# Performance work log

Measured on AMD Instinct MI355X. Metric: run time of the kernel, lower is better.

The kernel has to match this reference:

```python
import jax, jax.numpy as jnp
import numpy as np

GROUP = 128  # int4 quant group size and Hadamard block size

# Sylvester Hadamard matrix of size 128, orthonormal (H @ H.T = I)
_h = np.array([[1.0]], dtype=np.float32)
while _h.shape[0] < GROUP:
    _h = np.kron(_h, np.array([[1.0, 1.0], [1.0, -1.0]], dtype=np.float32))
H128 = jnp.asarray(_h / np.sqrt(GROUP))


def hadamard_rotate(x):
    # blockwise Hadamard rotation along the last dim (last dim % 128 == 0)
    *lead, n = x.shape
    xr = x.reshape(*lead, n // GROUP, GROUP) @ H128
    return xr.reshape(*lead, n)


def dequant_int4(wq, scales):
    # wq: [out, in] uint4 values in [0,16); scales: [out, in//GROUP]
    out_dim, in_dim = wq.shape
    w = (wq.astype(jnp.float32) - 8.0).reshape(out_dim, in_dim // GROUP, GROUP)
    w = w * scales[:, :, None]
    return w.reshape(out_dim, in_dim)


def rotate_linear_int4(x, wq, scales):
    # y = hadamard(x) @ dequant(W).T
    return hadamard_rotate(x) @ dequant_int4(wq, scales).T


def setup_inputs() -> dict:
    key = jax.random.key(0)
    ks = jax.random.split(key, 7)
    T, D, I = 4096, 4096, 12288  # tokens, hidden, intermediate
    x = jax.random.normal(ks[0], (T, D), dtype=jnp.float32)
    wq_gate = jax.random.randint(ks[1], (I, D), 0, 16, dtype=jnp.int32)
    s_gate = jax.random.uniform(ks[2], (I, D // GROUP), dtype=jnp.float32) * 0.01
    wq_up = jax.random.randint(ks[3], (I, D), 0, 16, dtype=jnp.int32)
    s_up = jax.random.uniform(ks[4], (I, D // GROUP), dtype=jnp.float32) * 0.01
    wq_down = jax.random.randint(ks[5], (D, I), 0, 16, dtype=jnp.int32)
    s_down = jax.random.uniform(ks[6], (D, I // GROUP), dtype=jnp.float32) * 0.01
    return {"x": x, "wq_gate": wq_gate, "s_gate": s_gate,
            "wq_up": wq_up, "s_up": s_up,
            "wq_down": wq_down, "s_down": s_down}


def reference(x, wq_gate, s_gate, wq_up, s_up, wq_down, s_down):
    gate = rotate_linear_int4(x, wq_gate, s_gate)   # [T, I]
    up = rotate_linear_int4(x, wq_up, s_up)         # [T, I]
    h = jax.nn.silu(gate) * up                       # SiluAndMul on cat([gate, up])
    return rotate_linear_int4(h, wq_down, s_down)    # [T, D]
```

## Files before the change

### kernel.cpp

```cpp
#include <hip/hip_runtime.h>
#include <hip/hip_bf16.h>
#include <cstdint>

#define T_DIM 4096
#define D_DIM 4096
#define I_DIM 12288
#define GRP   128

typedef __attribute__((ext_vector_type(8))) short bf16x8;
typedef __attribute__((ext_vector_type(4))) float f32x4;
typedef __attribute__((ext_vector_type(4))) int   int32x4;

typedef __attribute__((address_space(3))) void lds_void;
typedef const __attribute__((address_space(1))) void gmem_void;

static __device__ __forceinline__ unsigned short f2bf(float f) {
    unsigned int u = __float_as_uint(f);
    u += 0x7FFFu + ((u >> 16) & 1u);
    return (unsigned short)(u >> 16);
}
static __device__ __forceinline__ float bf2f(unsigned short b) {
    return __uint_as_float(((unsigned int)b) << 16);
}

__global__ void had_f32_to_bf16(const float* __restrict__ in, unsigned short* __restrict__ out,
                                int ngroups) {
    int gid = blockIdx.x * (blockDim.x >> 6) + (threadIdx.x >> 6);
    if (gid >= ngroups) return;
    int lane = threadIdx.x & 63;
    const float2 v2 = *reinterpret_cast<const float2*>(in + (size_t)gid * 128 + lane * 2);
    float v0 = v2.x, v1 = v2.y;
    { float t0 = v0 + v1, t1 = v0 - v1; v0 = t0; v1 = t1; }
#pragma unroll
    for (int m = 1; m <= 32; m <<= 1) {
        float b0 = __shfl_xor(v0, m);
        float b1 = __shfl_xor(v1, m);
        if (lane & m) { v0 = b0 - v0; v1 = b1 - v1; }
        else          { v0 = v0 + b0; v1 = v1 + b1; }
    }
    const float s = 0.08838834764831843f;
    unsigned int o = (unsigned int)f2bf(v0 * s) | ((unsigned int)f2bf(v1 * s) << 16);
    *reinterpret_cast<unsigned int*>(out + (size_t)gid * 128 + lane * 2) = o;
}

__global__ void had_bf16_inplace(unsigned short* __restrict__ buf, int ngroups) {
    int gid = blockIdx.x * (blockDim.x >> 6) + (threadIdx.x >> 6);
    if (gid >= ngroups) return;
    int lane = threadIdx.x & 63;
    unsigned int pv = *reinterpret_cast<const unsigned int*>(buf + (size_t)gid * 128 + lane * 2);
    float v0 = __uint_as_float((pv & 0xFFFFu) << 16);
    float v1 = __uint_as_float(pv & 0xFFFF0000u);
    { float t0 = v0 + v1, t1 = v0 - v1; v0 = t0; v1 = t1; }
#pragma unroll
    for (int m = 1; m <= 32; m <<= 1) {
        float b0 = __shfl_xor(v0, m);
        float b1 = __shfl_xor(v1, m);
        if (lane & m) { v0 = b0 - v0; v1 = b1 - v1; }
        else          { v0 = v0 + b0; v1 = v1 + b1; }
    }
    const float s = 0.08838834764831843f;
    unsigned int o = (unsigned int)f2bf(v0 * s) | ((unsigned int)f2bf(v1 * s) << 16);
    *reinterpret_cast<unsigned int*>(buf + (size_t)gid * 128 + lane * 2) = o;
}

__global__ void dequant_w(const int* __restrict__ Wq, const float* __restrict__ S,
                          unsigned short* __restrict__ Wbf, int In, int total8) {
    int t = blockIdx.x * blockDim.x + threadIdx.x;
    if (t >= total8) return;
    size_t base = (size_t)t * 8;
    size_t row = base / (size_t)In;
    int col = (int)(base - row * (size_t)In);
    float sc = S[row * (size_t)(In >> 7) + (col >> 7)];
    const int32x4* p = reinterpret_cast<const int32x4*>(Wq + base);
    int32x4 a = p[0], b = p[1];
    float nsc = -8.0f * sc;
    unsigned int o0 = (unsigned int)f2bf((float)a.x * sc + nsc) |
                      ((unsigned int)f2bf((float)a.y * sc + nsc) << 16);
    unsigned int o1 = (unsigned int)f2bf((float)a.z * sc + nsc) |
                      ((unsigned int)f2bf((float)a.w * sc + nsc) << 16);
    unsigned int o2 = (unsigned int)f2bf((float)b.x * sc + nsc) |
                      ((unsigned int)f2bf((float)b.y * sc + nsc) << 16);
    unsigned int o3 = (unsigned int)f2bf((float)b.z * sc + nsc) |
                      ((unsigned int)f2bf((float)b.w * sc + nsc) << 16);
    *reinterpret_cast<uint4*>(Wbf + base) = make_uint4(o0, o1, o2, o3);
}


#define GBAR()  __builtin_amdgcn_s_barrier()
#define LGKM0() asm volatile("s_waitcnt lgkmcnt(0)" ::: "memory")
#define VMW(n)  asm volatile("s_waitcnt vmcnt(" #n ")" ::: "memory")
#define P1()    __builtin_amdgcn_s_setprio(1)
#define P0()    __builtin_amdgcn_s_setprio(0)

#define STG(bb, mat, h, kb)                                                            \
  { _Pragma("unroll")                                                                  \
    for (int i_ = 0; i_ < 2; ++i_) {                                                   \
      const int rl_ = (h) * 128 + i_ * 64 + (tid >> 3);                                \
      const int gs_ = (tid & 7) ^ ((tid >> 3) & 7);                                    \
      const unsigned short* gp_ = ((mat) ? W : A) +                                    \
          (size_t)(((mat) ? n0 : m0) + rl_) * K + (kb) + gs_ * 8;                      \
      unsigned short* lp_ = lds + (bb) * 32768 + (mat) * 16384 +                       \
          ((h) * 128 + i_ * 64 + wid * 8) * 64;                                        \
      __builtin_amdgcn_global_load_lds((gmem_void*)gp_, (lds_void*)lp_, 16, 0, 0);     \
    } }

#define LDA(bb, q)                                                                     \
  _Pragma("unroll")                                                                    \
  for (int mi_ = 0; mi_ < 2; ++mi_)                                                    \
  _Pragma("unroll")                                                                    \
  for (int ks_ = 0; ks_ < 2; ++ks_) {                                                  \
    int r_ = wr * 128 + ((q) * 2 + mi_) * 16 + (lane & 15);                            \
    int c_ = ks_ * 4 + kc;                                                             \
    af[mi_][ks_] = *reinterpret_cast<const bf16x8*>(                                   \
        lds + (bb) * 32768 + r_ * 64 + ((c_ ^ (r_ & 7)) << 3));                        \
  }

#define LDB(bb)                                                                        \
  _Pragma("unroll")                                                                    \
  for (int ni_ = 0; ni_ < 4; ++ni_)                                                    \
  _Pragma("unroll")                                                                    \
  for (int ks_ = 0; ks_ < 2; ++ks_) {                                                  \
    int r_ = wc * 64 + ni_ * 16 + (lane & 15);                                         \
    int c_ = ks_ * 4 + kc;                                                             \
    bk[ni_][ks_] = *reinterpret_cast<const bf16x8*>(                                   \
        lds + (bb) * 32768 + 16384 + r_ * 64 + ((c_ ^ (r_ & 7)) << 3));                \
  }

#define MF16(q)                                                                        \
  _Pragma("unroll")                                                                    \
  for (int ks_ = 0; ks_ < 2; ++ks_)                                                    \
  _Pragma("unroll")                                                                    \
  for (int mi_ = 0; mi_ < 2; ++mi_)                                                    \
  _Pragma("unroll")                                                                    \
  for (int ni_ = 0; ni_ < 4; ++ni_)                                                    \
    acc[(q) * 2 + mi_][ni_] = __builtin_amdgcn_mfma_f32_16x16x32_bf16(                 \
        af[mi_][ks_], bk[ni_][ks_], acc[(q) * 2 + mi_][ni_], 0, 0, 0);

template<int MODE>
__global__ __launch_bounds__(512, 2)
void gemm256(const unsigned short* __restrict__ A,
             const unsigned short* __restrict__ W,
             void* __restrict__ C, int M, int N, int K)
{
    __shared__ __align__(16) unsigned short lds[65536];

    const int MT = M >> 8;
    const int nwg = gridDim.x;
    const int bid = blockIdx.x;
    const int cpx = nwg >> 3;
    const int wg  = (bid & 7) * cpx + (bid >> 3);
    const int m0 = (wg % MT) << 8;
    const int n0 = (wg / MT) << 8;

    const int tid  = threadIdx.x;
    const int lane = tid & 63;
    const int wid  = tid >> 6;
    const int wr = wid >> 2;
    const int wc = wid & 3;
    const int kc = lane >> 4;

    f32x4 acc[8][4];
#pragma unroll
    for (int i = 0; i < 8; ++i)
#pragma unroll
        for (int j = 0; j < 4; ++j) acc[i][j] = (f32x4)0.0f;

    const int NT = K >> 6;
    const int J  = NT >> 1;

    STG(0, 0, 0, 0); STG(0, 0, 1, 0); STG(0, 1, 0, 0); STG(0, 1, 1, 0);
    STG(1, 1, 0, 64); STG(1, 1, 1, 64);
    VMW(4);
    GBAR();

    bf16x8 af[2][2], bk[4][2];

    for (int j = 0; j < J - 1; ++j) {
        const int ka  = (j << 7);
        const int kb1 = ka + 64;
        const int ka2 = ka + 128;
        const int ka3 = ka + 192;
        LDB(0); LDA(0, 0); STG(1, 0, 0, kb1);
        GBAR(); LGKM0(); P1(); MF16(0); P0(); GBAR();
        LDA(0, 1); STG(1, 0, 1, kb1);
        GBAR(); LGKM0(); P1(); MF16(1); P0(); GBAR();
        LDA(0, 2); STG(0, 1, 0, ka2);
        GBAR(); LGKM0(); P1(); MF16(2); P0(); GBAR();
        LDA(0, 3); STG(0, 1, 1, ka2);
        GBAR(); LGKM0(); P1(); MF16(3); P0(); VMW(4); GBAR();
        LDB(1); LDA(1, 0); STG(0, 0, 0, ka2);
        GBAR(); LGKM0(); P1(); MF16(0); P0(); GBAR();
        LDA(1, 1); STG(0, 0, 1, ka2);
        GBAR(); LGKM0(); P1(); MF16(1); P0(); GBAR();
        LDA(1, 2); STG(1, 1, 0, ka3);
        GBAR(); LGKM0(); P1(); MF16(2); P0(); GBAR();
        LDA(1, 3); STG(1, 1, 1, ka3);
        GBAR(); LGKM0(); P1(); MF16(3); P0(); VMW(4); GBAR();
    }

    {
        const int kb1 = ((NT - 1) << 6);
        LDB(0); LDA(0, 0); STG(1, 0, 0, kb1);
        GBAR(); LGKM0(); P1(); MF16(0); P0(); GBAR();
        LDA(0, 1); STG(1, 0, 1, kb1);
        GBAR(); LGKM0(); P1(); MF16(1); P0(); GBAR();
        LDA(0, 2);
        GBAR(); LGKM0(); P1(); MF16(2); P0(); GBAR();
        LDA(0, 3);
        GBAR(); LGKM0(); P1(); MF16(3); P0(); VMW(0); GBAR();
        LDB(1); LDA(1, 0);
        GBAR(); LGKM0(); P1(); MF16(0); P0(); GBAR();
        LDA(1, 1);
        GBAR(); LGKM0(); P1(); MF16(1); P0(); GBAR();
        LDA(1, 2);
        GBAR(); LGKM0(); P1(); MF16(2); P0(); GBAR();
        LDA(1, 3);
        GBAR(); LGKM0(); P1(); MF16(3); P0(); GBAR();
    }

#pragma unroll
    for (int mi = 0; mi < 8; ++mi)
#pragma unroll
        for (int ni = 0; ni < 4; ++ni) {
            const int col = n0 + (wc << 6) + ni * 16 + (lane & 15);
#pragma unroll
            for (int r = 0; r < 4; ++r) {
                const int row = m0 + (wr << 7) + mi * 16 + ((lane >> 4) << 2) + r;
                const size_t idx = (size_t)row * N + col;
                if (MODE == 2) {
                    ((float*)C)[idx] = acc[mi][ni][r];
                } else if (MODE == 0) {
                    ((unsigned short*)C)[idx] = f2bf(acc[mi][ni][r]);
                } else {
                    float g = bf2f(((unsigned short*)C)[idx]);
                    float u = acc[mi][ni][r];
                    float h = (g / (1.0f + __expf(-g))) * u;
                    ((unsigned short*)C)[idx] = f2bf(h);
                }
            }
        }
}

__global__ __launch_bounds__(256, 2)
void gemm_gateup_fb(const unsigned short* __restrict__ Xr,
                    const int* __restrict__ Wg, const float* __restrict__ Sg,
                    const int* __restrict__ Wu, const float* __restrict__ Su,
                    unsigned short* __restrict__ H)
{
    __shared__ __align__(16) unsigned short lA [128 * 64];
    __shared__ __align__(16) unsigned short lBg[128 * 64];
    __shared__ __align__(16) unsigned short lBu[128 * 64];
    const int MT = T_DIM / 128;
    const int bid = blockIdx.x;
    const int m0 = (bid % MT) * 128;
    const int n0 = (bid / MT) * 128;
    const int tid  = threadIdx.x;
    const int lane = tid & 63;
    const int wid  = tid >> 6;
    const int wr = wid >> 1, wc = wid & 1;
    f32x4 accG[4][4], accU[4][4];
#pragma unroll
    for (int i = 0; i < 4; ++i)
#pragma unroll
        for (int j = 0; j < 4; ++j) { accG[i][j] = (f32x4)0.0f; accU[i][j] = (f32x4)0.0f; }
    const int arow = lane >> 3;
    const int acol = (lane & 7) * 8;
    const int SStride = D_DIM / GRP;
    for (int k0 = 0; k0 < D_DIM; k0 += 64) {
        __syncthreads();
#pragma unroll
        for (int it = 0; it < 4; ++it) {
            int chunk = wid * 4 + it;
            const unsigned short* gp = Xr + (size_t)(m0 + chunk * 8 + arow) * D_DIM + k0 + acol;
            __builtin_amdgcn_global_load_lds((gmem_void*)gp, (lds_void*)(lA + chunk * 512), 16, 0, 0);
        }
        const int g = k0 >> 7;
#pragma unroll
        for (int i = 0; i < 8; ++i) {
            int linear = i * 1024 + tid * 4;
            int r = linear >> 6;
            int c = linear & 63;
            const int32x4 wg = *reinterpret_cast<const int32x4*>(Wg + (size_t)(n0 + r) * D_DIM + k0 + c);
            const int32x4 wu = *reinterpret_cast<const int32x4*>(Wu + (size_t)(n0 + r) * D_DIM + k0 + c);
            float scg = Sg[(size_t)(n0 + r) * SStride + g];
            float scu = Su[(size_t)(n0 + r) * SStride + g];
            unsigned int g01 = (unsigned int)f2bf((float)(wg.x - 8) * scg) | ((unsigned int)f2bf((float)(wg.y - 8) * scg) << 16);
            unsigned int g23 = (unsigned int)f2bf((float)(wg.z - 8) * scg) | ((unsigned int)f2bf((float)(wg.w - 8) * scg) << 16);
            unsigned int u01 = (unsigned int)f2bf((float)(wu.x - 8) * scu) | ((unsigned int)f2bf((float)(wu.y - 8) * scu) << 16);
            unsigned int u23 = (unsigned int)f2bf((float)(wu.z - 8) * scu) | ((unsigned int)f2bf((float)(wu.w - 8) * scu) << 16);
            *reinterpret_cast<uint2*>(lBg + r * 64 + c) = make_uint2(g01, g23);
            *reinterpret_cast<uint2*>(lBu + r * 64 + c) = make_uint2(u01, u23);
        }
        __syncthreads();
#pragma unroll
        for (int ks = 0; ks < 2; ++ks) {
            const int koff = ks * 32 + (lane >> 4) * 8;
            bf16x8 af[4], bg[4], bu[4];
#pragma unroll
            for (int mi = 0; mi < 4; ++mi)
                af[mi] = *reinterpret_cast<const bf16x8*>(lA + (wr * 64 + mi * 16 + (lane & 15)) * 64 + koff);
#pragma unroll
            for (int ni = 0; ni < 4; ++ni) {
                bg[ni] = *reinterpret_cast<const bf16x8*>(lBg + (wc * 64 + ni * 16 + (lane & 15)) * 64 + koff);
                bu[ni] = *reinterpret_cast<const bf16x8*>(lBu + (wc * 64 + ni * 16 + (lane & 15)) * 64 + koff);
            }
#pragma unroll
            for (int mi = 0; mi < 4; ++mi)
#pragma unroll
                for (int ni = 0; ni < 4; ++ni) {
                    accG[mi][ni] = __builtin_amdgcn_mfma_f32_16x16x32_bf16(af[mi], bg[ni], accG[mi][ni], 0, 0, 0);
                    accU[mi][ni] = __builtin_amdgcn_mfma_f32_16x16x32_bf16(af[mi], bu[ni], accU[mi][ni], 0, 0, 0);
                }
        }
    }
#pragma unroll
    for (int mi = 0; mi < 4; ++mi)
#pragma unroll
        for (int ni = 0; ni < 4; ++ni) {
            const int col = n0 + wc * 64 + ni * 16 + (lane & 15);
#pragma unroll
            for (int r = 0; r < 4; ++r) {
                const int row = m0 + wr * 64 + mi * 16 + (lane >> 4) * 4 + r;
                float gv = accG[mi][ni][r];
                float uv = accU[mi][ni][r];
                float hv = (gv / (1.0f + __expf(-gv))) * uv;
                H[(size_t)row * I_DIM + col] = f2bf(hv);
            }
        }
}

__global__ __launch_bounds__(256, 2)
void gemm_down_fb(const unsigned short* __restrict__ Hr,
                  const int* __restrict__ Wd, const float* __restrict__ Sd,
                  float* __restrict__ Out)
{
    __shared__ __align__(16) unsigned short lA[128 * 64];
    __shared__ __align__(16) unsigned short lB[128 * 64];
    const int MT = T_DIM / 128;
    const int bid = blockIdx.x;
    const int m0 = (bid % MT) * 128;
    const int n0 = (bid / MT) * 128;
    const int tid  = threadIdx.x;
    const int lane = tid & 63;
    const int wid  = tid >> 6;
    const int wr = wid >> 1, wc = wid & 1;
    f32x4 acc[4][4];
#pragma unroll
    for (int i = 0; i < 4; ++i)
#pragma unroll
        for (int j = 0; j < 4; ++j) acc[i][j] = (f32x4)0.0f;
    const int arow = lane >> 3;
    const int acol = (lane & 7) * 8;
    const int SStride = I_DIM / GRP;
    for (int k0 = 0; k0 < I_DIM; k0 += 64) {
        __syncthreads();
#pragma unroll
        for (int it = 0; it < 4; ++it) {
            int chunk = wid * 4 + it;
            const unsigned short* gp = Hr + (size_t)(m0 + chunk * 8 + arow) * I_DIM + k0 + acol;
            __builtin_amdgcn_global_load_lds((gmem_void*)gp, (lds_void*)(lA + chunk * 512), 16, 0, 0);
        }
        const int g = k0 >> 7;
#pragma unroll
        for (int i = 0; i < 8; ++i) {
            int linear = i * 1024 + tid * 4;
            int r = linear >> 6;
            int c = linear & 63;
            const int32x4 wd = *reinterpret_cast<const int32x4*>(Wd + (size_t)(n0 + r) * I_DIM + k0 + c);
            float sc = Sd[(size_t)(n0 + r) * SStride + g];
            unsigned int d01 = (unsigned int)f2bf((float)(wd.x - 8) * sc) | ((unsigned int)f2bf((float)(wd.y - 8) * sc) << 16);
            unsigned int d23 = (unsigned int)f2bf((float)(wd.z - 8) * sc) | ((unsigned int)f2bf((float)(wd.w - 8) * sc) << 16);
            *reinterpret_cast<uint2*>(lB + r * 64 + c) = make_uint2(d01, d23);
        }
        __syncthreads();
#pragma unroll
        for (int ks = 0; ks < 2; ++ks) {
            const int koff = ks * 32 + (lane >> 4) * 8;
            bf16x8 af[4], bfr[4];
#pragma unroll
            for (int mi = 0; mi < 4; ++mi)
                af[mi] = *reinterpret_cast<const bf16x8*>(lA + (wr * 64 + mi * 16 + (lane & 15)) * 64 + koff);
#pragma unroll
            for (int ni = 0; ni < 4; ++ni)
                bfr[ni] = *reinterpret_cast<const bf16x8*>(lB + (wc * 64 + ni * 16 + (lane & 15)) * 64 + koff);
#pragma unroll
            for (int mi = 0; mi < 4; ++mi)
#pragma unroll
                for (int ni = 0; ni < 4; ++ni)
                    acc[mi][ni] = __builtin_amdgcn_mfma_f32_16x16x32_bf16(af[mi], bfr[ni], acc[mi][ni], 0, 0, 0);
        }
    }
#pragma unroll
    for (int mi = 0; mi < 4; ++mi)
#pragma unroll
        for (int ni = 0; ni < 4; ++ni) {
            const int col = n0 + wc * 64 + ni * 16 + (lane & 15);
#pragma unroll
            for (int r = 0; r < 4; ++r) {
                const int row = m0 + wr * 64 + mi * 16 + (lane >> 4) * 4 + r;
                Out[(size_t)row * D_DIM + col] = acc[mi][ni][r];
            }
        }
}

extern "C" void kernel_launch(void* const* d_in, const int* in_sizes, int n_in,
                              void* d_out, int out_size, void* d_ws, size_t ws_size,
                              hipStream_t stream) {
    const float* x       = (const float*)d_in[0];
    const int*   wq_gate = (const int*)d_in[1];
    const float* s_gate  = (const float*)d_in[2];
    const int*   wq_up   = (const int*)d_in[3];
    const float* s_up    = (const float*)d_in[4];
    const int*   wq_down = (const int*)d_in[5];
    const float* s_down  = (const float*)d_in[6];
    float* out = (float*)d_out;

    const size_t XR_E = (size_t)T_DIM * D_DIM;
    const size_t H_E  = (size_t)T_DIM * I_DIM;
    const size_t W_E  = (size_t)I_DIM * D_DIM;
    const size_t need = (XR_E + H_E + 2 * W_E) * sizeof(unsigned short);

    unsigned short* xr = (unsigned short*)d_ws;
    unsigned short* h  = xr + XR_E;

    {
        int ngroups = (int)(XR_E / 128);
        had_f32_to_bf16<<<dim3(ngroups / 4), dim3(256), 0, stream>>>(x, xr, ngroups);
    }

    if (ws_size >= need) {
        unsigned short* wgbf = h + H_E;
        unsigned short* wubf = wgbf + W_E;
        int total8 = (int)(W_E / 8);
        dequant_w<<<dim3((total8 + 255) / 256), dim3(256), 0, stream>>>(wq_gate, s_gate, wgbf, D_DIM, total8);
        dequant_w<<<dim3((total8 + 255) / 256), dim3(256), 0, stream>>>(wq_up,   s_up,   wubf, D_DIM, total8);
        gemm256<0><<<dim3((T_DIM / 256) * (I_DIM / 256)), dim3(512), 0, stream>>>(
            xr, wgbf, (void*)h, T_DIM, I_DIM, D_DIM);
        gemm256<1><<<dim3((T_DIM / 256) * (I_DIM / 256)), dim3(512), 0, stream>>>(
            xr, wubf, (void*)h, T_DIM, I_DIM, D_DIM);
        {
            int ngroups = (int)(H_E / 128);
            had_bf16_inplace<<<dim3(ngroups / 4), dim3(256), 0, stream>>>(h, ngroups);
        }
        dequant_w<<<dim3((total8 + 255) / 256), dim3(256), 0, stream>>>(wq_down, s_down, wgbf, I_DIM, total8);
        gemm256<2><<<dim3((T_DIM / 256) * (D_DIM / 256)), dim3(512), 0, stream>>>(
            h, wgbf, (void*)out, T_DIM, D_DIM, I_DIM);
    } else {
        gemm_gateup_fb<<<dim3((T_DIM / 128) * (I_DIM / 128)), dim3(256), 0, stream>>>(
            xr, wq_gate, s_gate, wq_up, s_up, h);
        {
            int ngroups = (int)(H_E / 128);
            had_bf16_inplace<<<dim3(ngroups / 4), dim3(256), 0, stream>>>(h, ngroups);
        }
        gemm_down_fb<<<dim3((T_DIM / 128) * (D_DIM / 128)), dim3(256), 0, stream>>>(
            h, wq_down, s_down, out);
    }
}
```

Baseline: 1.280 ms.

## Triple-buffer A tiles in LDS and drop explicit lgkmcnt waits in GEMM pipeline

Restructures the bf16 GEMM main loop so the A operand rotates through three LDS buffers while B keeps two, with staging loads issued earlier to deepen the prefetch distance. The explicit lgkmcnt(0) waits and several barriers per sub-step are removed, leaving the compiler to insert LDS waits, and the peeled tail iteration is folded into the loop behind a predicate. LDS use grows from 128KB to 160KB per workgroup, which may cut occupancy below the declared two blocks per CU, and the reduced barrier count raises the risk of LDS reuse races.

```diff
diff --git a/kernel.cpp b/kernel.cpp
--- a/kernel.cpp
+++ b/kernel.cpp
@@ -87,35 +87,33 @@
 
 
 #define GBAR()  __builtin_amdgcn_s_barrier()
-#define LGKM0() asm volatile("s_waitcnt lgkmcnt(0)" ::: "memory")
+#define FENCE() asm volatile("" ::: "memory")
 #define VMW(n)  asm volatile("s_waitcnt vmcnt(" #n ")" ::: "memory")
 #define P1()    __builtin_amdgcn_s_setprio(1)
 #define P0()    __builtin_amdgcn_s_setprio(0)
 
-#define STG(bb, mat, h, kb)                                                            \
+#define STG(src, row0, base, h, kb)                                                    \
   { _Pragma("unroll")                                                                  \
     for (int i_ = 0; i_ < 2; ++i_) {                                                   \
       const int rl_ = (h) * 128 + i_ * 64 + (tid >> 3);                                \
       const int gs_ = (tid & 7) ^ ((tid >> 3) & 7);                                    \
-      const unsigned short* gp_ = ((mat) ? W : A) +                                    \
-          (size_t)(((mat) ? n0 : m0) + rl_) * K + (kb) + gs_ * 8;                      \
-      unsigned short* lp_ = lds + (bb) * 32768 + (mat) * 16384 +                       \
-          ((h) * 128 + i_ * 64 + wid * 8) * 64;                                        \
+      const unsigned short* gp_ = (src) + (size_t)((row0) + rl_) * K + (kb) + gs_ * 8; \
+      unsigned short* lp_ = lds + (base) + ((h) * 128 + i_ * 64 + wid * 8) * 64;       \
       __builtin_amdgcn_global_load_lds((gmem_void*)gp_, (lds_void*)lp_, 16, 0, 0);     \
     } }
 
-#define LDA(bb, q)                                                                     \
+#define LDA(base, q)                                                                   \
   _Pragma("unroll")                                                                    \
   for (int mi_ = 0; mi_ < 2; ++mi_)                                                    \
   _Pragma("unroll")                                                                    \
   for (int ks_ = 0; ks_ < 2; ++ks_) {                                                  \
-    int r_ = wr * 128 + ((q) * 2 + mi_) * 16 + (lane & 15);                            \
+    int r_ = wr * 128 + (q) * 32 + mi_ * 16 + (lane & 15);                             \
     int c_ = ks_ * 4 + kc;                                                             \
     af[mi_][ks_] = *reinterpret_cast<const bf16x8*>(                                   \
-        lds + (bb) * 32768 + r_ * 64 + ((c_ ^ (r_ & 7)) << 3));                        \
+        lds + (base) + r_ * 64 + ((c_ ^ (r_ & 7)) << 3));                              \
   }
 
-#define LDB(bb)                                                                        \
+#define LDB(base)                                                                      \
   _Pragma("unroll")                                                                    \
   for (int ni_ = 0; ni_ < 4; ++ni_)                                                    \
   _Pragma("unroll")                                                                    \
@@ -123,7 +121,7 @@
     int r_ = wc * 64 + ni_ * 16 + (lane & 15);                                         \
     int c_ = ks_ * 4 + kc;                                                             \
     bk[ni_][ks_] = *reinterpret_cast<const bf16x8*>(                                   \
-        lds + (bb) * 32768 + 16384 + r_ * 64 + ((c_ ^ (r_ & 7)) << 3));                \
+        lds + (base) + r_ * 64 + ((c_ ^ (r_ & 7)) << 3));                              \
   }
 
 #define MF16(q)                                                                        \
@@ -135,6 +133,9 @@
   for (int ni_ = 0; ni_ < 4; ++ni_)                                                    \
     acc[(q) * 2 + mi_][ni_] = __builtin_amdgcn_mfma_f32_16x16x32_bf16(                 \
         af[mi_][ks_], bk[ni_][ks_], acc[(q) * 2 + mi_][ni_], 0, 0, 0);
+
+#define B0_ 49152
+#define B1_ 65536
 
 template<int MODE>
 __global__ __launch_bounds__(512, 2)
@@ -142,7 +143,7 @@
              const unsigned short* __restrict__ W,
              void* __restrict__ C, int M, int N, int K)
 {
-    __shared__ __align__(16) unsigned short lds[65536];
+    __shared__ __align__(16) unsigned short lds[81920];
 
     const int MT = M >> 8;
     const int nwg = gridDim.x;
@@ -168,54 +169,53 @@
     const int NT = K >> 6;
     const int J  = NT >> 1;
 
-    STG(0, 0, 0, 0); STG(0, 0, 1, 0); STG(0, 1, 0, 0); STG(0, 1, 1, 0);
-    STG(1, 1, 0, 64); STG(1, 1, 1, 64);
-    VMW(4);
-    GBAR();
-
-    bf16x8 af[2][2], bk[4][2];
-
-    for (int j = 0; j < J - 1; ++j) {
-        const int ka  = (j << 7);
-        const int kb1 = ka + 64;
-        const int ka2 = ka + 128;
-        const int ka3 = ka + 192;
-        LDB(0); LDA(0, 0); STG(1, 0, 0, kb1);
-        GBAR(); LGKM0(); P1(); MF16(0); P0(); GBAR();
-        LDA(0, 1); STG(1, 0, 1, kb1);
-        GBAR(); LGKM0(); P1(); MF16(1); P0(); GBAR();
-        LDA(0, 2); STG(0, 1, 0, ka2);
-        GBAR(); LGKM0(); P1(); MF16(2); P0(); GBAR();
-        LDA(0, 3); STG(0, 1, 1, ka2);
-        GBAR(); LGKM0(); P1(); MF16(3); P0(); VMW(4); GBAR();
-        LDB(1); LDA(1, 0); STG(0, 0, 0, ka2);
-        GBAR(); LGKM0(); P1(); MF16(0); P0(); GBAR();
-        LDA(1, 1); STG(0, 0, 1, ka2);
-        GBAR(); LGKM0(); P1(); MF16(1); P0(); GBAR();
-        LDA(1, 2); STG(1, 1, 0, ka3);
-        GBAR(); LGKM0(); P1(); MF16(2); P0(); GBAR();
-        LDA(1, 3); STG(1, 1, 1, ka3);
-        GBAR(); LGKM0(); P1(); MF16(3); P0(); VMW(4); GBAR();
-    }
-
-    {
-        const int kb1 = ((NT - 1) << 6);
-        LDB(0); LDA(0, 0); STG(1, 0, 0, kb1);
-        GBAR(); LGKM0(); P1(); MF16(0); P0(); GBAR();
-        LDA(0, 1); STG(1, 0, 1, kb1);
-        GBAR(); LGKM0(); P1(); MF16(1); P0(); GBAR();
-        LDA(0, 2);
-        GBAR(); LGKM0(); P1(); MF16(2); P0(); GBAR();
-        LDA(0, 3);
-        GBAR(); LGKM0(); P1(); MF16(3); P0(); VMW(0); GBAR();
-        LDB(1); LDA(1, 0);
-        GBAR(); LGKM0(); P1(); MF16(0); P0(); GBAR();
-        LDA(1, 1);
-        GBAR(); LGKM0(); P1(); MF16(1); P0(); GBAR();
-        LDA(1, 2);
-        GBAR(); LGKM0(); P1(); MF16(2); P0(); GBAR();
-        LDA(1, 3);
-        GBAR(); LGKM0(); P1(); MF16(3); P0(); GBAR();
+    STG(A, m0, 0,     0, 0);  STG(A, m0, 0,     1, 0);
+    STG(W, n0, B0_,   0, 0);  STG(W, n0, B0_,   1, 0);
+    STG(A, m0, 16384, 0, 64); STG(A, m0, 16384, 1, 64);
+    STG(W, n0, B1_,   0, 64);
+    VMW(6);
+    GBAR(); FENCE();
+
+    int ra = 0, rb = 1, rc = 2;
+
+    for (int j = 0; j < J; ++j) {
+        const bool st = (j < J - 1);
+        const int a   = j << 1;
+        const int kT1 = (a + 1) << 6;
+        const int kT2 = (a + 2) << 6;
+        const int kT3 = (a + 3) << 6;
+        const int baA = ra << 14, bbA = rb << 14, bcA = rc << 14;
+        bf16x8 af[2][2], bk[4][2];
+
+        STG(W, n0, B1_, 1, kT1);
+        LDB(B0_); LDA(baA, 0);
+        P1(); MF16(0); P0(); GBAR(); FENCE();
+        if (st) STG(A, m0, bcA, 0, kT2);
+        LDA(baA, 1);
+        P1(); MF16(1); P0(); GBAR(); FENCE();
+        if (st) STG(W, n0, B0_, 0, kT2);
+        LDA(baA, 2);
+        P1(); MF16(2); P0(); GBAR(); FENCE();
+        if (st) STG(W, n0, B0_, 1, kT2);
+        LDA(baA, 3);
+        P1(); MF16(3); P0();
+        if (st) { VMW(6); } else { VMW(0); }
+        GBAR(); FENCE();
+        if (st) STG(A, m0, bcA, 1, kT2);
+        LDB(B1_); LDA(bbA, 0);
+        P1(); MF16(0); P0(); GBAR(); FENCE();
+        if (st) STG(A, m0, baA, 0, kT3);
+        LDA(bbA, 1);
+        P1(); MF16(1); P0(); GBAR(); FENCE();
+        if (st) STG(A, m0, baA, 1, kT3);
+        LDA(bbA, 2);
+        P1(); MF16(2); P0(); GBAR(); FENCE();
+        if (st) STG(W, n0, B1_, 0, kT3);
+        LDA(bbA, 3);
+        P1(); MF16(3); P0();
+        if (st) { VMW(6); }
+        GBAR(); FENCE();
+        int t_ = ra; ra = rc; rc = rb; rb = t_;
     }
 
 #pragma unroll
```

Result: no change. 1.302 ms (+1.7%).

## Double-buffer A fragments in registers to prefetch the next LDS quarter during MFMA

Applied to the files above, without the earlier changes.

The GEMM main loop now keeps two register sets of A fragments and loads the next quarter tile from LDS while the MFMAs for the current quarter run. The explicit lgkmcnt(0) waits are removed, so the compiler's dependency-based waits can let LDS reads overlap with matrix math. The prologue now waits for the first stage and preloads the first A quarter. The vmcnt waits are moved to just before reads of the other LDS buffer. Those reads now come right after the wait with no barrier in between, which risks a race with other waves' async loads, and the extra fragment registers raise register pressure.

```diff
diff --git a/kernel.cpp b/kernel.cpp
--- a/kernel.cpp
+++ b/kernel.cpp
@@ -87,7 +87,6 @@
 
 
 #define GBAR()  __builtin_amdgcn_s_barrier()
-#define LGKM0() asm volatile("s_waitcnt lgkmcnt(0)" ::: "memory")
 #define VMW(n)  asm volatile("s_waitcnt vmcnt(" #n ")" ::: "memory")
 #define P1()    __builtin_amdgcn_s_setprio(1)
 #define P0()    __builtin_amdgcn_s_setprio(0)
@@ -104,18 +103,18 @@
       __builtin_amdgcn_global_load_lds((gmem_void*)gp_, (lds_void*)lp_, 16, 0, 0);     \
     } }
 
-#define LDA(bb, q)                                                                     \
+#define LDAQ(dst, bb, q)                                                               \
   _Pragma("unroll")                                                                    \
   for (int mi_ = 0; mi_ < 2; ++mi_)                                                    \
   _Pragma("unroll")                                                                    \
   for (int ks_ = 0; ks_ < 2; ++ks_) {                                                  \
-    int r_ = wr * 128 + ((q) * 2 + mi_) * 16 + (lane & 15);                            \
+    int r_ = wr * 128 + (q) * 32 + mi_ * 16 + (lane & 15);                             \
     int c_ = ks_ * 4 + kc;                                                             \
-    af[mi_][ks_] = *reinterpret_cast<const bf16x8*>(                                   \
+    dst[mi_][ks_] = *reinterpret_cast<const bf16x8*>(                                  \
         lds + (bb) * 32768 + r_ * 64 + ((c_ ^ (r_ & 7)) << 3));                        \
   }
 
-#define LDB(bb)                                                                        \
+#define LDBQ(bb)                                                                       \
   _Pragma("unroll")                                                                    \
   for (int ni_ = 0; ni_ < 4; ++ni_)                                                    \
   _Pragma("unroll")                                                                    \
@@ -126,7 +125,7 @@
         lds + (bb) * 32768 + 16384 + r_ * 64 + ((c_ ^ (r_ & 7)) << 3));                \
   }
 
-#define MF16(q)                                                                        \
+#define MF16(q, afb)                                                                   \
   _Pragma("unroll")                                                                    \
   for (int ks_ = 0; ks_ < 2; ++ks_)                                                    \
   _Pragma("unroll")                                                                    \
@@ -134,7 +133,7 @@
   _Pragma("unroll")                                                                    \
   for (int ni_ = 0; ni_ < 4; ++ni_)                                                    \
     acc[(q) * 2 + mi_][ni_] = __builtin_amdgcn_mfma_f32_16x16x32_bf16(                 \
-        af[mi_][ks_], bk[ni_][ks_], acc[(q) * 2 + mi_][ni_], 0, 0, 0);
+        afb[mi_][ks_], bk[ni_][ks_], acc[(q) * 2 + mi_][ni_], 0, 0, 0);
 
 template<int MODE>
 __global__ __launch_bounds__(512, 2)
@@ -168,54 +167,55 @@
     const int NT = K >> 6;
     const int J  = NT >> 1;
 
-    STG(0, 0, 0, 0); STG(0, 0, 1, 0); STG(0, 1, 0, 0); STG(0, 1, 1, 0);
+    bf16x8 afA[2][2], afB[2][2], bk[4][2];
+
+    STG(0, 0, 0, 0); STG(0, 0, 1, 0);
+    STG(0, 1, 0, 0); STG(0, 1, 1, 0);
+    VMW(0);
+    GBAR();
+    LDAQ(afA, 0, 0);
     STG(1, 1, 0, 64); STG(1, 1, 1, 64);
-    VMW(4);
-    GBAR();
-
-    bf16x8 af[2][2], bk[4][2];
 
     for (int j = 0; j < J - 1; ++j) {
         const int ka  = (j << 7);
         const int kb1 = ka + 64;
         const int ka2 = ka + 128;
         const int ka3 = ka + 192;
-        LDB(0); LDA(0, 0); STG(1, 0, 0, kb1);
-        GBAR(); LGKM0(); P1(); MF16(0); P0(); GBAR();
-        LDA(0, 1); STG(1, 0, 1, kb1);
-        GBAR(); LGKM0(); P1(); MF16(1); P0(); GBAR();
-        LDA(0, 2); STG(0, 1, 0, ka2);
-        GBAR(); LGKM0(); P1(); MF16(2); P0(); GBAR();
-        LDA(0, 3); STG(0, 1, 1, ka2);
-        GBAR(); LGKM0(); P1(); MF16(3); P0(); VMW(4); GBAR();
-        LDB(1); LDA(1, 0); STG(0, 0, 0, ka2);
-        GBAR(); LGKM0(); P1(); MF16(0); P0(); GBAR();
-        LDA(1, 1); STG(0, 0, 1, ka2);
-        GBAR(); LGKM0(); P1(); MF16(1); P0(); GBAR();
-        LDA(1, 2); STG(1, 1, 0, ka3);
-        GBAR(); LGKM0(); P1(); MF16(2); P0(); GBAR();
-        LDA(1, 3); STG(1, 1, 1, ka3);
-        GBAR(); LGKM0(); P1(); MF16(3); P0(); VMW(4); GBAR();
+        LDBQ(0); LDAQ(afB, 0, 1); STG(1, 0, 0, kb1);
+        GBAR(); P1(); MF16(0, afA); P0(); GBAR();
+        LDAQ(afA, 0, 2); STG(1, 0, 1, kb1);
+        GBAR(); P1(); MF16(1, afB); P0(); GBAR();
+        LDAQ(afB, 0, 3); STG(0, 1, 0, ka2);
+        GBAR(); P1(); MF16(2, afA); P0(); GBAR();
+        VMW(2); LDAQ(afA, 1, 0); STG(0, 1, 1, ka2);
+        GBAR(); P1(); MF16(3, afB); P0(); GBAR();
+        LDBQ(1); LDAQ(afB, 1, 1); STG(0, 0, 0, ka2);
+        GBAR(); P1(); MF16(0, afA); P0(); GBAR();
+        LDAQ(afA, 1, 2); STG(0, 0, 1, ka2);
+        GBAR(); P1(); MF16(1, afB); P0(); GBAR();
+        LDAQ(afB, 1, 3); STG(1, 1, 0, ka3);
+        GBAR(); P1(); MF16(2, afA); P0(); GBAR();
+        VMW(2); LDAQ(afA, 0, 0); STG(1, 1, 1, ka3);
+        GBAR(); P1(); MF16(3, afB); P0(); GBAR();
     }
 
     {
         const int kb1 = ((NT - 1) << 6);
-        LDB(0); LDA(0, 0); STG(1, 0, 0, kb1);
-        GBAR(); LGKM0(); P1(); MF16(0); P0(); GBAR();
-        LDA(0, 1); STG(1, 0, 1, kb1);
-        GBAR(); LGKM0(); P1(); MF16(1); P0(); GBAR();
-        LDA(0, 2);
-        GBAR(); LGKM0(); P1(); MF16(2); P0(); GBAR();
-        LDA(0, 3);
-        GBAR(); LGKM0(); P1(); MF16(3); P0(); VMW(0); GBAR();
-        LDB(1); LDA(1, 0);
-        GBAR(); LGKM0(); P1(); MF16(0); P0(); GBAR();
-        LDA(1, 1);
-        GBAR(); LGKM0(); P1(); MF16(1); P0(); GBAR();
-        LDA(1, 2);
-        GBAR(); LGKM0(); P1(); MF16(2); P0(); GBAR();
-        LDA(1, 3);
-        GBAR(); LGKM0(); P1(); MF16(3); P0(); GBAR();
+        LDBQ(0); LDAQ(afB, 0, 1); STG(1, 0, 0, kb1);
+        GBAR(); P1(); MF16(0, afA); P0(); GBAR();
+        LDAQ(afA, 0, 2); STG(1, 0, 1, kb1);
+        GBAR(); P1(); MF16(1, afB); P0(); GBAR();
+        LDAQ(afB, 0, 3);
+        GBAR(); P1(); MF16(2, afA); P0(); GBAR();
+        VMW(0); LDAQ(afA, 1, 0);
+        GBAR(); P1(); MF16(3, afB); P0(); GBAR();
+        LDBQ(1); LDAQ(afB, 1, 1);
+        GBAR(); P1(); MF16(0, afA); P0(); GBAR();
+        LDAQ(afA, 1, 2);
+        GBAR(); P1(); MF16(1, afB); P0(); GBAR();
+        LDAQ(afB, 1, 3);
+        GBAR(); P1(); MF16(2, afA); P0(); GBAR();
+        GBAR(); P1(); MF16(3, afB); P0();
     }
 
 #pragma unroll
```

New measurement: 1.278 ms. No clear change (-0.1%).
